# Kernel optimization log

Measured on AMD Instinct MI355X. Metric: run time of the kernel, lower is better.

The kernel has to match this reference:

```python
import jax, jax.numpy as jnp
import numpy as np
from jax import lax

# DeepSeek-V3 noaux_tc routing config (scaled expert MLPs)
E = 256            # n_routed_experts
N_GROUP = 8
TOPK_GROUP = 4
TOP_K = 8          # num_experts_per_tok
SCALE = 2.5        # routed_scaling_factor
H = 1024           # hidden_size
I = 256            # moe_intermediate_size
T = 256            # batch*seq tokens


def setup_inputs() -> dict:
    key = jax.random.key(0)
    ks = jax.random.split(key, 9)
    s_h = 1.0 / np.sqrt(H)
    s_i = 1.0 / np.sqrt(I)
    return {
        "hidden_states": jax.random.normal(ks[0], (1, 1, T, H), jnp.float32),
        "gate_w": jax.random.normal(ks[1], (E, H), jnp.float32) * s_h,
        "e_bias": jax.random.normal(ks[2], (E,), jnp.float32) * 0.1,
        "w_gate": jax.random.normal(ks[3], (E, H, I), jnp.float32) * s_h,
        "w_up": jax.random.normal(ks[4], (E, H, I), jnp.float32) * s_h,
        "w_down": jax.random.normal(ks[5], (E, I, H), jnp.float32) * s_i,
        "sw_gate": jax.random.normal(ks[6], (H, I), jnp.float32) * s_h,
        "sw_up": jax.random.normal(ks[7], (H, I), jnp.float32) * s_h,
        "sw_down": jax.random.normal(ks[8], (I, H), jnp.float32) * s_i,
    }


def reference(hidden_states, gate_w, e_bias, w_gate, w_up, w_down,
              sw_gate, sw_up, sw_down):
    x = hidden_states.reshape(-1, H)                      # [T, H]
    t = x.shape[0]

    # ---- gate: sigmoid scores + correction bias, grouped top-k ----
    logits = x @ gate_w.T                                  # [T, E]
    scores = jax.nn.sigmoid(logits)
    sc = scores + e_bias                                   # corrected scores

    grouped = sc.reshape(t, N_GROUP, E // N_GROUP)         # [T, G, E/G]
    group_scores = lax.top_k(grouped, 2)[0].sum(-1)        # top-2 per group summed [T, G]
    group_idx = lax.top_k(group_scores, TOPK_GROUP)[1]     # [T, topk_group]
    group_mask = jnp.zeros_like(group_scores).at[
        jnp.arange(t)[:, None], group_idx].set(1.0)        # [T, G]
    expert_mask = jnp.repeat(group_mask, E // N_GROUP, axis=-1)  # [T, E]

    masked = jnp.where(expert_mask > 0, sc, -jnp.inf)
    topk_idx = lax.top_k(masked, TOP_K)[1]                 # [T, k]
    topk_w = jnp.take_along_axis(scores, topk_idx, axis=-1)  # weights from raw scores
    topk_w = topk_w / (topk_w.sum(-1, keepdims=True) + 1e-20) * SCALE

    # combine matrix: [T, E], dense-equivalent of dispatch/recall
    combine = (jax.nn.one_hot(topk_idx, E, dtype=x.dtype)
               * topk_w[..., None]).sum(axis=1)

    # ---- routed experts (dense reference for all-to-all dispatch) ----
    h1 = jnp.einsum('th,ehi->eti', x, w_gate)              # [E, T, I]
    h3 = jnp.einsum('th,ehi->eti', x, w_up)
    eo = jnp.einsum('eti,eih->eth', jax.nn.silu(h1) * h3, w_down)  # [E, T, H]
    y = jnp.einsum('eth,te->th', eo, combine)              # weighted recall

    # ---- shared expert (always active) ----
    shared = (jax.nn.silu(x @ sw_gate) * (x @ sw_up)) @ sw_down

    return (y + shared).reshape(hidden_states.shape)
```

## Files before the change

### kernel.cpp

```cpp
#include <hip/hip_runtime.h>
#include <math.h>

#define T 256
#define E 256
#define H 1024
#define I_DIM 256
#define CAP 256
#define NPASS 16

__global__ __launch_bounds__(256) void k1_logits(
    const float* __restrict__ x, const float* __restrict__ gw,
    float* __restrict__ logits, int* __restrict__ cnt, float* __restrict__ out)
{
    const int t = blockIdx.x, j = threadIdx.x;
    __shared__ __align__(16) float xs[H];
#pragma unroll
    for (int k = 0; k < 4; ++k) xs[k * 256 + j] = x[t * H + k * 256 + j];
#pragma unroll
    for (int k = 0; k < 4; ++k) out[t * H + k * 256 + j] = 0.f;
    if (t == 0) cnt[j] = 0;
    __syncthreads();
    const float4* w4 = (const float4*)(gw + (size_t)j * H);
    const float4* x4 = (const float4*)xs;
    float acc = 0.f;
#pragma unroll 8
    for (int h = 0; h < H / 4; ++h) {
        float4 w = w4[h];
        float4 v = x4[h];
        acc = fmaf(w.x, v.x, acc);
        acc = fmaf(w.y, v.y, acc);
        acc = fmaf(w.z, v.z, acc);
        acc = fmaf(w.w, v.w, acc);
    }
    logits[t * E + j] = acc;
}

__global__ __launch_bounds__(64) void k2_route(
    const float* __restrict__ logits, const float* __restrict__ e_bias,
    int* __restrict__ cnt, int* __restrict__ tok, float* __restrict__ wt)
{
    const int t = blockIdx.x;
    const int lane = threadIdx.x;

    float s[4], sc[4];
#pragma unroll
    for (int q = 0; q < 4; ++q) {
        int e = lane * 4 + q;
        float l = logits[t * E + e];
        float sig = 1.f / (1.f + expf(-l));
        s[q] = sig;
        sc[q] = sig + e_bias[e];
    }

    float m01 = fmaxf(sc[0], sc[1]), n01 = fminf(sc[0], sc[1]);
    float m23 = fmaxf(sc[2], sc[3]), n23 = fminf(sc[2], sc[3]);
    float a1 = fmaxf(m01, m23);
    float a2 = fmaxf(fminf(m01, m23), fmaxf(n01, n23));
#pragma unroll
    for (int off = 1; off < 8; off <<= 1) {
        float b1 = __shfl_xor(a1, off);
        float b2 = __shfl_xor(a2, off);
        float na1 = fmaxf(a1, b1);
        float na2 = fmaxf(fminf(a1, b1), fmaxf(a2, b2));
        a1 = na1; a2 = na2;
    }
    float gs = a1 + a2;

    __shared__ float gsc[8];
    if ((lane & 7) == 0) gsc[lane >> 3] = gs;
    __syncthreads();

    float lg[8];
#pragma unroll
    for (int g = 0; g < 8; ++g) lg[g] = gsc[g];
    unsigned gmask = 0;
#pragma unroll
    for (int k = 0; k < 4; ++k) {
        float best = -__builtin_inff(); int bi = 0;
#pragma unroll
        for (int g = 0; g < 8; ++g) {
            bool take = !((gmask >> g) & 1u) && (lg[g] > best);
            if (take) { best = lg[g]; bi = g; }
        }
        gmask |= 1u << bi;
    }

    bool gon = (gmask >> (lane >> 3)) & 1u;
    float masked[4];
#pragma unroll
    for (int q = 0; q < 4; ++q) masked[q] = gon ? sc[q] : -__builtin_inff();

    int sel[8]; float selw[8]; float wsum = 0.f;
#pragma unroll
    for (int k = 0; k < 8; ++k) {
        float v = masked[0]; int qi = 0;
#pragma unroll
        for (int q = 1; q < 4; ++q) { if (masked[q] > v) { v = masked[q]; qi = q; } }
        int idx = lane * 4 + qi;
#pragma unroll
        for (int off = 1; off < 64; off <<= 1) {
            float ov = __shfl_xor(v, off);
            int   oi = __shfl_xor(idx, off);
            if (ov > v || (ov == v && oi < idx)) { v = ov; idx = oi; }
        }
        float rawv = s[idx & 3];
        rawv = __shfl(rawv, idx >> 2);
        sel[k] = idx; selw[k] = rawv; wsum += rawv;
        if ((idx >> 2) == lane) masked[idx & 3] = -__builtin_inff();
    }
    float scale = 2.5f / (wsum + 1e-20f);

#pragma unroll
    for (int k = 0; k < 8; ++k) {
        if (lane == k) {
            int e = sel[k];
            int pos = atomicAdd(&cnt[e], 1);
            tok[e * CAP + pos] = t;
            wt[e * CAP + pos] = selw[k] * scale;
        }
    }
}

__global__ __launch_bounds__(256) void k3_experts(
    const float* __restrict__ x,
    const float* __restrict__ w_gate, const float* __restrict__ w_up,
    const float* __restrict__ w_down,
    const float* __restrict__ swg, const float* __restrict__ swu,
    const float* __restrict__ swd,
    const int* __restrict__ cnt, const int* __restrict__ tok,
    const float* __restrict__ wt, float* __restrict__ out)
{
    const int b = blockIdx.x;
    const int j = threadIdx.x;

    __shared__ __align__(16) float smem[16 * 256];
    __shared__ int   stok[16];
    __shared__ float swt_s[16];

    const float *wg, *wu, *wd;
    int nn;

    if (b < 16) {
        if (j < 16) { stok[j] = b * 16 + j; swt_s[j] = 1.f; }
        wg = swg; wu = swu; wd = swd;
        nn = 16;
    } else {
        const int rb = b - 16;
        const int e = rb & 255;
        const int p = rb >> 8;
        const int n = cnt[e];
        const int base = p * 16;
        if (base >= n) return;
        nn = min(16, n - base);
        if (j < 16) {
            int tg = base + j;
            bool valid = tg < n;
            stok[j] = valid ? tok[e * CAP + tg] : tok[e * CAP + base];
            swt_s[j] = valid ? wt[e * CAP + tg] : 0.f;
        }
        wg = w_gate + (size_t)e * H * I_DIM;
        wu = w_up   + (size_t)e * H * I_DIM;
        wd = w_down + (size_t)e * I_DIM * H;
    }

    float h1[16], h3[16];
#pragma unroll
    for (int t2 = 0; t2 < 16; ++t2) { h1[t2] = 0.f; h3[t2] = 0.f; }

    for (int h0 = 0; h0 < H; h0 += 256) {
        __syncthreads();
#pragma unroll
        for (int t2 = 0; t2 < 16; ++t2)
            smem[t2 * 256 + j] = x[(size_t)stok[t2] * H + h0 + j];
        __syncthreads();
#pragma unroll 1
        for (int hh = 0; hh < 256; hh += 16) {
            float wa[16], wb[16];
#pragma unroll
            for (int u = 0; u < 16; ++u)
                wa[u] = wg[(size_t)(h0 + hh + u) * I_DIM + j];
#pragma unroll
            for (int u = 0; u < 16; ++u)
                wb[u] = wu[(size_t)(h0 + hh + u) * I_DIM + j];
#pragma unroll
            for (int t2 = 0; t2 < 16; ++t2) {
                float xv[16];
                *(float4*)&xv[0]  = *(const float4*)&smem[t2 * 256 + hh];
                *(float4*)&xv[4]  = *(const float4*)&smem[t2 * 256 + hh + 4];
                *(float4*)&xv[8]  = *(const float4*)&smem[t2 * 256 + hh + 8];
                *(float4*)&xv[12] = *(const float4*)&smem[t2 * 256 + hh + 12];
#pragma unroll
                for (int u = 0; u < 16; ++u)
                    h1[t2] = fmaf(xv[u], wa[u], h1[t2]);
#pragma unroll
                for (int u = 0; u < 16; ++u)
                    h3[t2] = fmaf(xv[u], wb[u], h3[t2]);
            }
        }
    }
    __syncthreads();
#pragma unroll
    for (int t2 = 0; t2 < 16; ++t2) {
        float v1 = h1[t2];
        float act = v1 / (1.f + __expf(-v1)) * h3[t2];
        smem[t2 * 256 + j] = act;
    }
    __syncthreads();
    for (int hblk = 0; hblk < 4; ++hblk) {
        float acc[16];
#pragma unroll
        for (int t2 = 0; t2 < 16; ++t2) acc[t2] = 0.f;
#pragma unroll 1
        for (int i = 0; i < I_DIM; i += 16) {
            float wv[16];
#pragma unroll
            for (int u = 0; u < 16; ++u)
                wv[u] = wd[(size_t)(i + u) * H + hblk * 256 + j];
#pragma unroll
            for (int t2 = 0; t2 < 16; ++t2) {
                float av[16];
                *(float4*)&av[0]  = *(const float4*)&smem[t2 * 256 + i];
                *(float4*)&av[4]  = *(const float4*)&smem[t2 * 256 + i + 4];
                *(float4*)&av[8]  = *(const float4*)&smem[t2 * 256 + i + 8];
                *(float4*)&av[12] = *(const float4*)&smem[t2 * 256 + i + 12];
#pragma unroll
                for (int u = 0; u < 16; ++u)
                    acc[t2] = fmaf(av[u], wv[u], acc[t2]);
            }
        }
#pragma unroll
        for (int t2 = 0; t2 < 16; ++t2) {
            if (t2 < nn)
                atomicAdd(&out[(size_t)stok[t2] * H + hblk * 256 + j],
                          swt_s[t2] * acc[t2]);
        }
    }
}

extern "C" void kernel_launch(void* const* d_in, const int* in_sizes, int n_in,
                              void* d_out, int out_size, void* d_ws, size_t ws_size,
                              hipStream_t stream) {
    const float* x      = (const float*)d_in[0];
    const float* gate_w = (const float*)d_in[1];
    const float* e_bias = (const float*)d_in[2];
    const float* w_gate = (const float*)d_in[3];
    const float* w_up   = (const float*)d_in[4];
    const float* w_down = (const float*)d_in[5];
    const float* swg    = (const float*)d_in[6];
    const float* swu    = (const float*)d_in[7];
    const float* swd    = (const float*)d_in[8];
    float* out = (float*)d_out;

    float* wsf = (float*)d_ws;
    float* logits = wsf;
    int*   cnt    = (int*)(wsf + 65536);
    int*   tok    = (int*)(wsf + 65792);
    float* wt     = wsf + 65792 + E * CAP;

    k1_logits<<<T, 256, 0, stream>>>(x, gate_w, logits, cnt, out);
    k2_route<<<T, 64, 0, stream>>>(logits, e_bias, cnt, tok, wt);
    k3_experts<<<16 + E * NPASS, 256, 0, stream>>>(
        x, w_gate, w_up, w_down, swg, swu, swd, cnt, tok, wt, out);
}
```

Before: 920.0 us.

## Fuse shared expert into logits kernel and double-buffer expert weight loads

The shared-expert MLP moves out of the expert kernel and into the per-token logits kernel, which now writes the output directly instead of zeroing it. The expert kernel now runs two blocks per expert: the first handles one 16-token chunk and the second loops over the rest. Weight rows are software-prefetched into alternating register sets so global loads overlap the FMA work, and launch bounds allow more registers per thread. The risks are higher register pressure, lower occupancy, and the cost of 256 token blocks each re-reading the full shared-expert weights from cache.

```diff
diff --git a/kernel.cpp b/kernel.cpp
--- a/kernel.cpp
+++ b/kernel.cpp
@@ -6,20 +6,21 @@
 #define H 1024
 #define I_DIM 256
 #define CAP 256
-#define NPASS 16
-
-__global__ __launch_bounds__(256) void k1_logits(
+
+__global__ __launch_bounds__(256) void k1_logits_shared(
     const float* __restrict__ x, const float* __restrict__ gw,
+    const float* __restrict__ swg, const float* __restrict__ swu,
+    const float* __restrict__ swd,
     float* __restrict__ logits, int* __restrict__ cnt, float* __restrict__ out)
 {
     const int t = blockIdx.x, j = threadIdx.x;
     __shared__ __align__(16) float xs[H];
+    __shared__ float act[I_DIM];
 #pragma unroll
     for (int k = 0; k < 4; ++k) xs[k * 256 + j] = x[t * H + k * 256 + j];
-#pragma unroll
-    for (int k = 0; k < 4; ++k) out[t * H + k * 256 + j] = 0.f;
     if (t == 0) cnt[j] = 0;
     __syncthreads();
+
     const float4* w4 = (const float4*)(gw + (size_t)j * H);
     const float4* x4 = (const float4*)xs;
     float acc = 0.f;
@@ -33,6 +34,31 @@
         acc = fmaf(w.w, v.w, acc);
     }
     logits[t * E + j] = acc;
+
+    float g = 0.f, uu = 0.f;
+#pragma unroll 8
+    for (int h = 0; h < H; ++h) {
+        float xv = xs[h];
+        g  = fmaf(xv, swg[h * I_DIM + j], g);
+        uu = fmaf(xv, swu[h * I_DIM + j], uu);
+    }
+    act[j] = g / (1.f + __expf(-g)) * uu;
+    __syncthreads();
+
+    float o0 = 0.f, o1 = 0.f, o2 = 0.f, o3 = 0.f;
+#pragma unroll 4
+    for (int i = 0; i < I_DIM; ++i) {
+        float a = act[i];
+        const float* wr = swd + (size_t)i * H;
+        o0 = fmaf(a, wr[j], o0);
+        o1 = fmaf(a, wr[256 + j], o1);
+        o2 = fmaf(a, wr[512 + j], o2);
+        o3 = fmaf(a, wr[768 + j], o3);
+    }
+    out[(size_t)t * H + j]       = o0;
+    out[(size_t)t * H + 256 + j] = o1;
+    out[(size_t)t * H + 512 + j] = o2;
+    out[(size_t)t * H + 768 + j] = o3;
 }
 
 __global__ __launch_bounds__(64) void k2_route(
@@ -121,119 +147,161 @@
     }
 }
 
-__global__ __launch_bounds__(256) void k3_experts(
+__global__ __launch_bounds__(256, 1) void k3_experts(
     const float* __restrict__ x,
     const float* __restrict__ w_gate, const float* __restrict__ w_up,
     const float* __restrict__ w_down,
-    const float* __restrict__ swg, const float* __restrict__ swu,
-    const float* __restrict__ swd,
     const int* __restrict__ cnt, const int* __restrict__ tok,
     const float* __restrict__ wt, float* __restrict__ out)
 {
-    const int b = blockIdx.x;
+    const int e = blockIdx.x & 255;
+    const int p = blockIdx.x >> 8;
     const int j = threadIdx.x;
+    const int n = cnt[e];
+    if (p * 16 >= n) return;
 
     __shared__ __align__(16) float smem[16 * 256];
     __shared__ int   stok[16];
     __shared__ float swt_s[16];
 
-    const float *wg, *wu, *wd;
-    int nn;
-
-    if (b < 16) {
-        if (j < 16) { stok[j] = b * 16 + j; swt_s[j] = 1.f; }
-        wg = swg; wu = swu; wd = swd;
-        nn = 16;
-    } else {
-        const int rb = b - 16;
-        const int e = rb & 255;
-        const int p = rb >> 8;
-        const int n = cnt[e];
-        const int base = p * 16;
-        if (base >= n) return;
-        nn = min(16, n - base);
+    const float* wg = w_gate + (size_t)e * H * I_DIM;
+    const float* wu = w_up   + (size_t)e * H * I_DIM;
+    const float* wd = w_down + (size_t)e * I_DIM * H;
+
+    for (int base = p * 16; base < n; base += 16) {
+        const int nn = min(16, n - base);
         if (j < 16) {
             int tg = base + j;
             bool valid = tg < n;
-            stok[j] = valid ? tok[e * CAP + tg] : tok[e * CAP + base];
+            stok[j]  = valid ? tok[e * CAP + tg] : tok[e * CAP + base];
             swt_s[j] = valid ? wt[e * CAP + tg] : 0.f;
         }
-        wg = w_gate + (size_t)e * H * I_DIM;
-        wu = w_up   + (size_t)e * H * I_DIM;
-        wd = w_down + (size_t)e * I_DIM * H;
-    }
-
-    float h1[16], h3[16];
-#pragma unroll
-    for (int t2 = 0; t2 < 16; ++t2) { h1[t2] = 0.f; h3[t2] = 0.f; }
-
-    for (int h0 = 0; h0 < H; h0 += 256) {
+
+        float h1[16], h3[16];
+#pragma unroll
+        for (int t2 = 0; t2 < 16; ++t2) { h1[t2] = 0.f; h3[t2] = 0.f; }
+
+        float wA[16], wB[16], wC[16], wD[16];
+#pragma unroll
+        for (int u = 0; u < 16; ++u) {
+            wA[u] = wg[(size_t)u * I_DIM + j];
+            wB[u] = wu[(size_t)u * I_DIM + j];
+        }
+
+        for (int h0 = 0; h0 < H; h0 += 256) {
+            __syncthreads();
+            {
+                const int t2 = j >> 4, c0 = (j & 15) * 16;
+                const float4* src = (const float4*)(x + (size_t)stok[t2] * H + h0 + c0);
+                float4* dst = (float4*)&smem[t2 * 256 + c0];
+                dst[0] = src[0]; dst[1] = src[1]; dst[2] = src[2]; dst[3] = src[3];
+            }
+            __syncthreads();
+#pragma unroll 1
+            for (int hh = 0; hh < 256; hh += 32) {
+                const int hB = h0 + hh + 16;
+                int hN = h0 + hh + 32;
+                if (hN >= H) hN = 0;
+#pragma unroll
+                for (int u = 0; u < 16; ++u) {
+                    wC[u] = wg[(size_t)(hB + u) * I_DIM + j];
+                    wD[u] = wu[(size_t)(hB + u) * I_DIM + j];
+                }
+#pragma unroll
+                for (int t2 = 0; t2 < 16; ++t2) {
+                    float xv[16];
+                    *(float4*)&xv[0]  = *(const float4*)&smem[t2 * 256 + hh];
+                    *(float4*)&xv[4]  = *(const float4*)&smem[t2 * 256 + hh + 4];
+                    *(float4*)&xv[8]  = *(const float4*)&smem[t2 * 256 + hh + 8];
+                    *(float4*)&xv[12] = *(const float4*)&smem[t2 * 256 + hh + 12];
+#pragma unroll
+                    for (int u = 0; u < 16; ++u) h1[t2] = fmaf(xv[u], wA[u], h1[t2]);
+#pragma unroll
+                    for (int u = 0; u < 16; ++u) h3[t2] = fmaf(xv[u], wB[u], h3[t2]);
+                }
+#pragma unroll
+                for (int u = 0; u < 16; ++u) {
+                    wA[u] = wg[(size_t)(hN + u) * I_DIM + j];
+                    wB[u] = wu[(size_t)(hN + u) * I_DIM + j];
+                }
+#pragma unroll
+                for (int t2 = 0; t2 < 16; ++t2) {
+                    float xv[16];
+                    *(float4*)&xv[0]  = *(const float4*)&smem[t2 * 256 + hh + 16];
+                    *(float4*)&xv[4]  = *(const float4*)&smem[t2 * 256 + hh + 20];
+                    *(float4*)&xv[8]  = *(const float4*)&smem[t2 * 256 + hh + 24];
+                    *(float4*)&xv[12] = *(const float4*)&smem[t2 * 256 + hh + 28];
+#pragma unroll
+                    for (int u = 0; u < 16; ++u) h1[t2] = fmaf(xv[u], wC[u], h1[t2]);
+#pragma unroll
+                    for (int u = 0; u < 16; ++u) h3[t2] = fmaf(xv[u], wD[u], h3[t2]);
+                }
+            }
+        }
         __syncthreads();
 #pragma unroll
-        for (int t2 = 0; t2 < 16; ++t2)
-            smem[t2 * 256 + j] = x[(size_t)stok[t2] * H + h0 + j];
+        for (int t2 = 0; t2 < 16; ++t2) {
+            float v1 = h1[t2];
+            smem[t2 * 256 + j] = v1 / (1.f + __expf(-v1)) * h3[t2];
+        }
         __syncthreads();
+
+        float acc[16];
+        float vA[16], vB[16];
+#pragma unroll
+        for (int u = 0; u < 16; ++u) vA[u] = wd[(size_t)u * H + j];
 #pragma unroll 1
-        for (int hh = 0; hh < 256; hh += 16) {
-            float wa[16], wb[16];
+        for (int c = 0; c < 64; c += 2) {
+            const int i0  = (c & 15) * 16;
+            const int hb0 = c >> 4;
+            const int c1 = c + 1;
+            const int i1  = (c1 & 15) * 16;
+            const int hb1 = c1 >> 4;
+            int c2 = c + 2; if (c2 >= 64) c2 = 0;
+            const int i2c = (c2 & 15) * 16;
+            const int hb2 = c2 >> 4;
+
+            if ((c & 15) == 0) {
+#pragma unroll
+                for (int t2 = 0; t2 < 16; ++t2) acc[t2] = 0.f;
+            }
 #pragma unroll
             for (int u = 0; u < 16; ++u)
-                wa[u] = wg[(size_t)(h0 + hh + u) * I_DIM + j];
-#pragma unroll
-            for (int u = 0; u < 16; ++u)
-                wb[u] = wu[(size_t)(h0 + hh + u) * I_DIM + j];
-#pragma unroll
-            for (int t2 = 0; t2 < 16; ++t2) {
-                float xv[16];
-                *(float4*)&xv[0]  = *(const float4*)&smem[t2 * 256 + hh];
-                *(float4*)&xv[4]  = *(const float4*)&smem[t2 * 256 + hh + 4];
-                *(float4*)&xv[8]  = *(const float4*)&smem[t2 * 256 + hh + 8];
-                *(float4*)&xv[12] = *(const float4*)&smem[t2 * 256 + hh + 12];
-#pragma unroll
-                for (int u = 0; u < 16; ++u)
-                    h1[t2] = fmaf(xv[u], wa[u], h1[t2]);
-#pragma unroll
-                for (int u = 0; u < 16; ++u)
-                    h3[t2] = fmaf(xv[u], wb[u], h3[t2]);
-            }
-        }
-    }
-    __syncthreads();
-#pragma unroll
-    for (int t2 = 0; t2 < 16; ++t2) {
-        float v1 = h1[t2];
-        float act = v1 / (1.f + __expf(-v1)) * h3[t2];
-        smem[t2 * 256 + j] = act;
-    }
-    __syncthreads();
-    for (int hblk = 0; hblk < 4; ++hblk) {
-        float acc[16];
-#pragma unroll
-        for (int t2 = 0; t2 < 16; ++t2) acc[t2] = 0.f;
-#pragma unroll 1
-        for (int i = 0; i < I_DIM; i += 16) {
-            float wv[16];
-#pragma unroll
-            for (int u = 0; u < 16; ++u)
-                wv[u] = wd[(size_t)(i + u) * H + hblk * 256 + j];
+                vB[u] = wd[(size_t)(i1 + u) * H + hb1 * 256 + j];
 #pragma unroll
             for (int t2 = 0; t2 < 16; ++t2) {
                 float av[16];
-                *(float4*)&av[0]  = *(const float4*)&smem[t2 * 256 + i];
-                *(float4*)&av[4]  = *(const float4*)&smem[t2 * 256 + i + 4];
-                *(float4*)&av[8]  = *(const float4*)&smem[t2 * 256 + i + 8];
-                *(float4*)&av[12] = *(const float4*)&smem[t2 * 256 + i + 12];
-#pragma unroll
-                for (int u = 0; u < 16; ++u)
-                    acc[t2] = fmaf(av[u], wv[u], acc[t2]);
-            }
-        }
-#pragma unroll
-        for (int t2 = 0; t2 < 16; ++t2) {
-            if (t2 < nn)
-                atomicAdd(&out[(size_t)stok[t2] * H + hblk * 256 + j],
-                          swt_s[t2] * acc[t2]);
-        }
+                *(float4*)&av[0]  = *(const float4*)&smem[t2 * 256 + i0];
+                *(float4*)&av[4]  = *(const float4*)&smem[t2 * 256 + i0 + 4];
+                *(float4*)&av[8]  = *(const float4*)&smem[t2 * 256 + i0 + 8];
+                *(float4*)&av[12] = *(const float4*)&smem[t2 * 256 + i0 + 12];
+#pragma unroll
+                for (int u = 0; u < 16; ++u) acc[t2] = fmaf(av[u], vA[u], acc[t2]);
+            }
+#pragma unroll
+            for (int u = 0; u < 16; ++u)
+                vA[u] = wd[(size_t)(i2c + u) * H + hb2 * 256 + j];
+#pragma unroll
+            for (int t2 = 0; t2 < 16; ++t2) {
+                float av[16];
+                *(float4*)&av[0]  = *(const float4*)&smem[t2 * 256 + i1];
+                *(float4*)&av[4]  = *(const float4*)&smem[t2 * 256 + i1 + 4];
+                *(float4*)&av[8]  = *(const float4*)&smem[t2 * 256 + i1 + 8];
+                *(float4*)&av[12] = *(const float4*)&smem[t2 * 256 + i1 + 12];
+#pragma unroll
+                for (int u = 0; u < 16; ++u) acc[t2] = fmaf(av[u], vB[u], acc[t2]);
+            }
+            if ((c1 & 15) == 15) {
+#pragma unroll
+                for (int t2 = 0; t2 < 16; ++t2) {
+                    if (t2 < nn)
+                        atomicAdd(&out[(size_t)stok[t2] * H + hb0 * 256 + j],
+                                  swt_s[t2] * acc[t2]);
+                }
+            }
+        }
+        if (p == 0) break;
+        __syncthreads();
     }
 }
 
@@ -257,8 +325,9 @@
     int*   tok    = (int*)(wsf + 65792);
     float* wt     = wsf + 65792 + E * CAP;
 
-    k1_logits<<<T, 256, 0, stream>>>(x, gate_w, logits, cnt, out);
+    k1_logits_shared<<<T, 256, 0, stream>>>(x, gate_w, swg, swu, swd,
+                                            logits, cnt, out);
     k2_route<<<T, 64, 0, stream>>>(logits, e_bias, cnt, tok, wt);
-    k3_experts<<<16 + E * NPASS, 256, 0, stream>>>(
-        x, w_gate, w_up, w_down, swg, swu, swd, cnt, tok, wt, out);
+    k3_experts<<<2 * E, 256, 0, stream>>>(
+        x, w_gate, w_up, w_down, cnt, tok, wt, out);
 }
```

After: 1.662 ms. +80.7%, slower.
